# Optimization experiments

Measured on AMD Instinct MI355X. Metric: run time of the kernel, lower is better.

Reference implementation:

```python
import jax, jax.numpy as jnp
import numpy as np

B, L, ENC_D, DEC_D, ATTN_D = 64, 1024, 512, 512, 512


def setup_inputs() -> dict:
    key = jax.random.key(0)
    ks = jax.random.split(key, 8)
    s_enc = 1.0 / np.sqrt(ENC_D)
    s_dec = 1.0 / np.sqrt(DEC_D)
    s_att = 1.0 / np.sqrt(ATTN_D)
    return {
        "enc_out": jax.random.normal(ks[0], (B, L, ENC_D), dtype=jnp.float32),
        "dec_hidden": jax.random.normal(ks[1], (B, DEC_D), dtype=jnp.float32),
        # nn.Linear params (uniform(-1/sqrt(fan_in), 1/sqrt(fan_in)))
        "W_enc": jax.random.uniform(ks[2], (ENC_D, ATTN_D), jnp.float32, -s_enc, s_enc),
        "b_enc": jax.random.uniform(ks[3], (ATTN_D,), jnp.float32, -s_enc, s_enc),
        "W_dec": jax.random.uniform(ks[4], (DEC_D, ATTN_D), jnp.float32, -s_dec, s_dec),
        "b_dec": jax.random.uniform(ks[5], (ATTN_D,), jnp.float32, -s_dec, s_dec),
        "W_full": jax.random.uniform(ks[6], (ATTN_D,), jnp.float32, -s_att, s_att),
        "b_full": jax.random.uniform(ks[7], (), jnp.float32, -s_att, s_att),
    }


def reference(enc_out, dec_hidden, W_enc, b_enc, W_dec, b_dec, W_full, b_full):
    # attn1: [B, L, A]; attn2: [B, A]
    attn1 = jnp.einsum("ble,ea->bla", enc_out, W_enc) + b_enc
    attn2 = dec_hidden @ W_dec + b_dec
    # full_attn(relu(attn1 + attn2[:, None])) -> [B, L]
    attn = jnp.einsum("bla,a->bl", jax.nn.relu(attn1 + attn2[:, None, :]), W_full) + b_full
    alpha = jax.nn.softmax(attn, axis=1)  # over L
    attn_weighted_enc = jnp.einsum("ble,bl->be", enc_out, alpha)
    return attn_weighted_enc, alpha
```

## Files before the change

kernel.cpp:

```cpp
#include <hip/hip_runtime.h>
#include <hip/hip_bf16.h>

typedef __bf16 bf16x8 __attribute__((ext_vector_type(8)));
typedef float f32x4 __attribute__((ext_vector_type(4)));
typedef unsigned int u32;

#define B_SZ 64
#define L_SZ 1024
#define D_SZ 512

#define WS_WT     0
#define WS_BIAS   524288
#define WS_LOGITS 655360
#define WS_PART   917504

__device__ __forceinline__ unsigned short f2bf(float f) {
    __bf16 h = (__bf16)f;
    return __builtin_bit_cast(unsigned short, h);
}

__device__ __forceinline__ void gload_lds16(const void* g, void* l) {
    __builtin_amdgcn_global_load_lds(
        (const __attribute__((address_space(1))) u32*)g,
        (__attribute__((address_space(3))) u32*)l, 16, 0, 0);
}

__global__ void k_wt(const float* __restrict__ W, unsigned short* __restrict__ Wt) {
    int n = blockIdx.x;
    for (int k = threadIdx.x; k < 512; k += 256)
        Wt[n * 512 + k] = f2bf(W[k * 512 + n]);
}

__global__ void k_bias2(const float* __restrict__ dec, const float* __restrict__ Wd,
                        const float* __restrict__ b_dec, const float* __restrict__ b_enc,
                        float* __restrict__ bias2p) {
    int blk = blockIdx.x;
    int b = blk >> 2, nc = blk & 3;
    int t = threadIdx.x;
    __shared__ float sdec[512];
    __shared__ float red[256];
    for (int k = t; k < 512; k += 256) sdec[k] = dec[b * 512 + k];
    __syncthreads();
    int n = nc * 128 + (t & 127);
    int kh = t >> 7;
    float acc = 0.f;
    int k0 = kh * 256;
    #pragma unroll 4
    for (int k = k0; k < k0 + 256; ++k)
        acc += sdec[k] * Wd[k * 512 + n];
    red[t] = acc;
    __syncthreads();
    if (t < 128) {
        int nn = nc * 128 + t;
        bias2p[b * 512 + nn] = red[t] + red[t + 128] + b_dec[nn] + b_enc[nn];
    }
}

__global__ __launch_bounds__(512, 4) void k_logits(
        const float* __restrict__ enc, const unsigned short* __restrict__ Wt,
        const float* __restrict__ bias2p, const float* __restrict__ Wf,
        const float* __restrict__ bfull, float* __restrict__ logits) {
    __shared__ __align__(16) unsigned short lds[2][8192];
    __shared__ f32x4 comb[4][2][64];

    int t = threadIdx.x;
    int lane = t & 63;
    int w = t >> 6;
    int rg = w >> 1;
    int h = w & 1;
    int blk = blockIdx.x;
    int b = blk >> 3;
    int m = lane & 15;
    int g = lane >> 4;

    #define STAGE(bufi, nc_)                                                      \
        {                                                                         \
            int n0_ = (nc_) * 16;                                                 \
            _Pragma("unroll")                                                     \
            for (int j = 0; j < 2; ++j) {                                         \
                int c_ = w * 2 + j;                                               \
                const char* src_ = (const char*)Wt + (size_t)(n0_ + c_) * 1024    \
                                   + ((lane ^ c_) << 4);                          \
                gload_lds16(src_, (char*)&lds[bufi][0] + c_ * 1024);              \
            }                                                                     \
        }

    STAGE(0, 0)

    bf16x8 A0[8], A1[8];
    {
        const float* ap0 = enc + (size_t)(blk * 128 + rg * 32 + m) * 512 + h * 256 + g * 8;
        const float* ap1 = ap0 + 16 * 512;
        #pragma unroll
        for (int f = 0; f < 8; ++f) {
            float4 x = *(const float4*)(ap0 + f * 32);
            float4 y = *(const float4*)(ap0 + f * 32 + 4);
            bf16x8 a;
            a[0] = (__bf16)x.x; a[1] = (__bf16)x.y; a[2] = (__bf16)x.z; a[3] = (__bf16)x.w;
            a[4] = (__bf16)y.x; a[5] = (__bf16)y.y; a[6] = (__bf16)y.z; a[7] = (__bf16)y.w;
            A0[f] = a;
            float4 x1 = *(const float4*)(ap1 + f * 32);
            float4 y1 = *(const float4*)(ap1 + f * 32 + 4);
            bf16x8 a1;
            a1[0] = (__bf16)x1.x; a1[1] = (__bf16)x1.y; a1[2] = (__bf16)x1.z; a1[3] = (__bf16)x1.w;
            a1[4] = (__bf16)y1.x; a1[5] = (__bf16)y1.y; a1[6] = (__bf16)y1.z; a1[7] = (__bf16)y1.w;
            A1[f] = a1;
        }
    }

    __syncthreads();

    float p0[4] = {0.f, 0.f, 0.f, 0.f};
    float p1[4] = {0.f, 0.f, 0.f, 0.f};
    int swz = m << 4;

    for (int nc = 0; nc < 32; ++nc) {
        int buf = nc & 1;
        if (nc < 31) {
            if (buf) STAGE(0, nc + 1) else STAGE(1, nc + 1)
        }
        const char* base = (const char*)&lds[buf][0] + m * 1024;
        f32x4 acc0 = {0.f, 0.f, 0.f, 0.f};
        f32x4 acc1 = {0.f, 0.f, 0.f, 0.f};
        #pragma unroll
        for (int f = 0; f < 8; ++f) {
            uint4 raw = *(const uint4*)(base + (((h * 8 + f) * 64 + g * 16) ^ swz));
            bf16x8 bfr = __builtin_bit_cast(bf16x8, raw);
            acc0 = __builtin_amdgcn_mfma_f32_16x16x32_bf16(A0[f], bfr, acc0, 0, 0, 0);
            acc1 = __builtin_amdgcn_mfma_f32_16x16x32_bf16(A1[f], bfr, acc1, 0, 0, 0);
        }
        if (h == 1) {
            comb[rg][0][lane] = acc0;
            comb[rg][1][lane] = acc1;
        }
        __syncthreads();
        if (h == 0) {
            f32x4 c0 = comb[rg][0][lane];
            f32x4 c1 = comb[rg][1][lane];
            int col = nc * 16 + m;
            float bias = bias2p[b * 512 + col];
            float wf = Wf[col];
            #pragma unroll
            for (int r = 0; r < 4; ++r) {
                float v0 = acc0[r] + c0[r] + bias; v0 = v0 > 0.f ? v0 : 0.f; p0[r] += v0 * wf;
                float v1 = acc1[r] + c1[r] + bias; v1 = v1 > 0.f ? v1 : 0.f; p1[r] += v1 * wf;
            }
        }
        __syncthreads();
    }

    if (h == 0) {
        float bf0 = bfull[0];
        int rowbase = blk * 128 + rg * 32;
        #pragma unroll
        for (int r = 0; r < 4; ++r) {
            float v = p0[r];
            v += __shfl_xor(v, 1, 64);
            v += __shfl_xor(v, 2, 64);
            v += __shfl_xor(v, 4, 64);
            v += __shfl_xor(v, 8, 64);
            if (m == 0) logits[rowbase + g * 4 + r] = v + bf0;
            float u = p1[r];
            u += __shfl_xor(u, 1, 64);
            u += __shfl_xor(u, 2, 64);
            u += __shfl_xor(u, 4, 64);
            u += __shfl_xor(u, 8, 64);
            if (m == 0) logits[rowbase + 16 + g * 4 + r] = u + bf0;
        }
    }
}

__global__ void k_softmax(const float* __restrict__ logits, float* __restrict__ alpha) {
    int b = blockIdx.x;
    int t = threadIdx.x;
    __shared__ float red[256];
    float4 v = ((const float4*)(logits + b * 1024))[t];
    float mx = fmaxf(fmaxf(v.x, v.y), fmaxf(v.z, v.w));
    red[t] = mx;
    __syncthreads();
    for (int s = 128; s > 0; s >>= 1) {
        if (t < s) red[t] = fmaxf(red[t], red[t + s]);
        __syncthreads();
    }
    mx = red[0];
    __syncthreads();
    float4 e;
    e.x = expf(v.x - mx); e.y = expf(v.y - mx);
    e.z = expf(v.z - mx); e.w = expf(v.w - mx);
    red[t] = e.x + e.y + e.z + e.w;
    __syncthreads();
    for (int s = 128; s > 0; s >>= 1) {
        if (t < s) red[t] += red[t + s];
        __syncthreads();
    }
    float inv = 1.0f / red[0];
    float4 o;
    o.x = e.x * inv; o.y = e.y * inv; o.z = e.z * inv; o.w = e.w * inv;
    ((float4*)(alpha + b * 1024))[t] = o;
}

__global__ void k_wsum_part(const float* __restrict__ enc, const float* __restrict__ alpha,
                            float* __restrict__ part) {
    int blk = blockIdx.x;
    int b = blk >> 3, c = blk & 7;
    int t = threadIdx.x;
    int col = (t & 127) * 4;
    int lh = t >> 7;
    const float* ep = enc + (size_t)(b * 1024 + c * 128) * 512;
    const float* al = alpha + b * 1024 + c * 128;
    float4 s = {0.f, 0.f, 0.f, 0.f};
    #pragma unroll 4
    for (int i = 0; i < 64; ++i) {
        int l = i * 2 + lh;
        float a = al[l];
        float4 e = *(const float4*)(ep + (size_t)l * 512 + col);
        s.x += e.x * a; s.y += e.y * a; s.z += e.z * a; s.w += e.w * a;
    }
    __shared__ float red[2][512];
    *(float4*)&red[lh][col] = s;
    __syncthreads();
    if (t < 128) {
        float4 a0 = *(const float4*)&red[0][t * 4];
        float4 a1 = *(const float4*)&red[1][t * 4];
        float4 o;
        o.x = a0.x + a1.x; o.y = a0.y + a1.y;
        o.z = a0.z + a1.z; o.w = a0.w + a1.w;
        *(float4*)(part + (size_t)blk * 512 + t * 4) = o;
    }
}

__global__ void k_wsum_final(const float* __restrict__ part, float* __restrict__ out) {
    int b = blockIdx.x;
    int t = threadIdx.x;
    float4 s = {0.f, 0.f, 0.f, 0.f};
    #pragma unroll
    for (int c = 0; c < 8; ++c) {
        float4 v = *(const float4*)(part + (size_t)(b * 8 + c) * 512 + t * 4);
        s.x += v.x; s.y += v.y; s.z += v.z; s.w += v.w;
    }
    *(float4*)(out + b * 512 + t * 4) = s;
}

extern "C" void kernel_launch(void* const* d_in, const int* in_sizes, int n_in,
                              void* d_out, int out_size, void* d_ws, size_t ws_size,
                              hipStream_t stream) {
    const float* enc    = (const float*)d_in[0];
    const float* dec    = (const float*)d_in[1];
    const float* W_enc  = (const float*)d_in[2];
    const float* b_enc  = (const float*)d_in[3];
    const float* W_dec  = (const float*)d_in[4];
    const float* b_dec  = (const float*)d_in[5];
    const float* W_full = (const float*)d_in[6];
    const float* b_full = (const float*)d_in[7];

    float* out = (float*)d_out;
    char* ws = (char*)d_ws;
    unsigned short* Wt = (unsigned short*)(ws + WS_WT);
    float* bias2p = (float*)(ws + WS_BIAS);
    float* logits = (float*)(ws + WS_LOGITS);
    float* part   = (float*)(ws + WS_PART);
    float* alpha  = out + 32768;

    hipLaunchKernelGGL(k_wt,         dim3(512), dim3(256), 0, stream, W_enc, Wt);
    hipLaunchKernelGGL(k_bias2,      dim3(256), dim3(256), 0, stream, dec, W_dec, b_dec, b_enc, bias2p);
    hipLaunchKernelGGL(k_logits,     dim3(512), dim3(512), 0, stream, enc, Wt, bias2p, W_full, b_full, logits);
    hipLaunchKernelGGL(k_softmax,    dim3(64),  dim3(256), 0, stream, logits, alpha);
    hipLaunchKernelGGL(k_wsum_part,  dim3(512), dim3(256), 0, stream, enc, alpha, part);
    hipLaunchKernelGGL(k_wsum_final, dim3(64),  dim3(128), 0, stream, part, out);
}
```

Measured before the change: 112.8 us.

## Halve logits block size and split epilogue work across both K-half waves

Result: faster. 110.5 us (-2.1%).

```diff
diff --git a/kernel.cpp b/kernel.cpp
--- a/kernel.cpp
+++ b/kernel.cpp
@@ -4,10 +4,6 @@
 typedef __bf16 bf16x8 __attribute__((ext_vector_type(8)));
 typedef float f32x4 __attribute__((ext_vector_type(4)));
 typedef unsigned int u32;
-
-#define B_SZ 64
-#define L_SZ 1024
-#define D_SZ 512
 
 #define WS_WT     0
 #define WS_BIAS   524288
@@ -56,12 +52,12 @@
     }
 }
 
-__global__ __launch_bounds__(512, 4) void k_logits(
+__global__ __launch_bounds__(256, 4) void k_logits(
         const float* __restrict__ enc, const unsigned short* __restrict__ Wt,
         const float* __restrict__ bias2p, const float* __restrict__ Wf,
-        const float* __restrict__ bfull, float* __restrict__ logits) {
+        float* __restrict__ logits) {
     __shared__ __align__(16) unsigned short lds[2][8192];
-    __shared__ f32x4 comb[4][2][64];
+    __shared__ f32x4 comb[2][2][64];
 
     int t = threadIdx.x;
     int lane = t & 63;
@@ -69,7 +65,7 @@
     int rg = w >> 1;
     int h = w & 1;
     int blk = blockIdx.x;
-    int b = blk >> 3;
+    int b = blk >> 4;
     int m = lane & 15;
     int g = lane >> 4;
 
@@ -77,8 +73,8 @@
         {                                                                         \
             int n0_ = (nc_) * 16;                                                 \
             _Pragma("unroll")                                                     \
-            for (int j = 0; j < 2; ++j) {                                         \
-                int c_ = w * 2 + j;                                               \
+            for (int j = 0; j < 4; ++j) {                                         \
+                int c_ = w * 4 + j;                                               \
                 const char* src_ = (const char*)Wt + (size_t)(n0_ + c_) * 1024    \
                                    + ((lane ^ c_) << 4);                          \
                 gload_lds16(src_, (char*)&lds[bufi][0] + c_ * 1024);              \
@@ -89,7 +85,7 @@
 
     bf16x8 A0[8], A1[8];
     {
-        const float* ap0 = enc + (size_t)(blk * 128 + rg * 32 + m) * 512 + h * 256 + g * 8;
+        const float* ap0 = enc + (size_t)(blk * 64 + rg * 32 + m) * 512 + h * 256 + g * 8;
         const float* ap1 = ap0 + 16 * 512;
         #pragma unroll
         for (int f = 0; f < 8; ++f) {
@@ -107,11 +103,13 @@
             A1[f] = a1;
         }
     }
-
-    __syncthreads();
-
-    float p0[4] = {0.f, 0.f, 0.f, 0.f};
-    float p1[4] = {0.f, 0.f, 0.f, 0.f};
+    #pragma unroll
+    for (int f = 0; f < 8; ++f)
+        asm volatile("" : "+v"(A0[f]), "+v"(A1[f]));
+
+    __syncthreads();
+
+    float p[4] = {0.f, 0.f, 0.f, 0.f};
     int swz = m << 4;
 
     for (int nc = 0; nc < 32; ++nc) {
@@ -129,44 +127,30 @@
             acc0 = __builtin_amdgcn_mfma_f32_16x16x32_bf16(A0[f], bfr, acc0, 0, 0, 0);
             acc1 = __builtin_amdgcn_mfma_f32_16x16x32_bf16(A1[f], bfr, acc1, 0, 0, 0);
         }
-        if (h == 1) {
-            comb[rg][0][lane] = acc0;
-            comb[rg][1][lane] = acc1;
-        }
-        __syncthreads();
-        if (h == 0) {
-            f32x4 c0 = comb[rg][0][lane];
-            f32x4 c1 = comb[rg][1][lane];
-            int col = nc * 16 + m;
-            float bias = bias2p[b * 512 + col];
-            float wf = Wf[col];
-            #pragma unroll
-            for (int r = 0; r < 4; ++r) {
-                float v0 = acc0[r] + c0[r] + bias; v0 = v0 > 0.f ? v0 : 0.f; p0[r] += v0 * wf;
-                float v1 = acc1[r] + c1[r] + bias; v1 = v1 > 0.f ? v1 : 0.f; p1[r] += v1 * wf;
-            }
-        }
-        __syncthreads();
-    }
-
-    if (h == 0) {
-        float bf0 = bfull[0];
-        int rowbase = blk * 128 + rg * 32;
+        comb[rg][h ^ 1][lane] = h ? acc0 : acc1;
+        __syncthreads();
+        f32x4 other = comb[rg][h][lane];
+        f32x4 own = h ? acc1 : acc0;
+        int col = nc * 16 + m;
+        float bias = bias2p[b * 512 + col];
+        float wf = Wf[col];
         #pragma unroll
         for (int r = 0; r < 4; ++r) {
-            float v = p0[r];
-            v += __shfl_xor(v, 1, 64);
-            v += __shfl_xor(v, 2, 64);
-            v += __shfl_xor(v, 4, 64);
-            v += __shfl_xor(v, 8, 64);
-            if (m == 0) logits[rowbase + g * 4 + r] = v + bf0;
-            float u = p1[r];
-            u += __shfl_xor(u, 1, 64);
-            u += __shfl_xor(u, 2, 64);
-            u += __shfl_xor(u, 4, 64);
-            u += __shfl_xor(u, 8, 64);
-            if (m == 0) logits[rowbase + 16 + g * 4 + r] = u + bf0;
-        }
+            float v = own[r] + other[r] + bias;
+            v = v > 0.f ? v : 0.f;
+            p[r] += v * wf;
+        }
+        __syncthreads();
+    }
+
+    #pragma unroll
+    for (int r = 0; r < 4; ++r) {
+        float v = p[r];
+        v += __shfl_xor(v, 1, 64);
+        v += __shfl_xor(v, 2, 64);
+        v += __shfl_xor(v, 4, 64);
+        v += __shfl_xor(v, 8, 64);
+        if (m == 0) logits[blk * 64 + rg * 32 + h * 16 + g * 4 + r] = v;
     }
 }
 
@@ -251,7 +235,6 @@
     const float* W_dec  = (const float*)d_in[4];
     const float* b_dec  = (const float*)d_in[5];
     const float* W_full = (const float*)d_in[6];
-    const float* b_full = (const float*)d_in[7];
 
     float* out = (float*)d_out;
     char* ws = (char*)d_ws;
@@ -261,10 +244,10 @@
     float* part   = (float*)(ws + WS_PART);
     float* alpha  = out + 32768;
 
-    hipLaunchKernelGGL(k_wt,         dim3(512), dim3(256), 0, stream, W_enc, Wt);
-    hipLaunchKernelGGL(k_bias2,      dim3(256), dim3(256), 0, stream, dec, W_dec, b_dec, b_enc, bias2p);
-    hipLaunchKernelGGL(k_logits,     dim3(512), dim3(512), 0, stream, enc, Wt, bias2p, W_full, b_full, logits);
-    hipLaunchKernelGGL(k_softmax,    dim3(64),  dim3(256), 0, stream, logits, alpha);
-    hipLaunchKernelGGL(k_wsum_part,  dim3(512), dim3(256), 0, stream, enc, alpha, part);
-    hipLaunchKernelGGL(k_wsum_final, dim3(64),  dim3(128), 0, stream, part, out);
-}
+    hipLaunchKernelGGL(k_wt,         dim3(512),  dim3(256), 0, stream, W_enc, Wt);
+    hipLaunchKernelGGL(k_bias2,      dim3(256),  dim3(256), 0, stream, dec, W_dec, b_dec, b_enc, bias2p);
+    hipLaunchKernelGGL(k_logits,     dim3(1024), dim3(256), 0, stream, enc, Wt, bias2p, W_full, logits);
+    hipLaunchKernelGGL(k_softmax,    dim3(64),   dim3(256), 0, stream, logits, alpha);
+    hipLaunchKernelGGL(k_wsum_part,  dim3(512),  dim3(256), 0, stream, enc, alpha, part);
+    hipLaunchKernelGGL(k_wsum_final, dim3(64),   dim3(128), 0, stream, part, out);
+}
```
